# Optimization experiments

Measured on AMD Instinct MI355X. Metric: run time of the kernel, lower is better.

The kernel has to match this reference:

```python
import jax, jax.numpy as jnp
import numpy as np

N = 128  # n_hidden == n_inputs == n_outputs
TWO_PI = 2.0 * np.pi


def build_unitary(mzi_phases, output_phases):
    """Clements mesh: n layers of disjoint 2x2 MZI rotations, composed left-to-right.
    Within a layer the MZIs act on disjoint pairs, so their product equals one dense
    layer matrix (matches the sequential torch loop exactly)."""
    n = N
    U = jnp.eye(n, dtype=jnp.complex64)
    idx = 0
    for layer in range(n):
        pi = np.arange(layer % 2, n - 1, 2)  # left indices of pairs this layer
        m = len(pi)
        theta = mzi_phases[idx:idx + 2 * m:2]
        phi = mzi_phases[idx + 1:idx + 2 * m:2]
        idx += 2 * m
        ct = jnp.cos(theta).astype(jnp.complex64)
        st = jnp.sin(theta).astype(jnp.complex64)
        ep = jnp.exp(1j * phi.astype(jnp.complex64))
        L = jnp.eye(n, dtype=jnp.complex64)
        L = L.at[pi, pi].set(ct * ep)
        L = L.at[pi, pi + 1].set(st)
        L = L.at[pi + 1, pi].set(st)
        L = L.at[pi + 1, pi + 1].set(-ct * jnp.conj(ep))
        U = U @ L
    return U * jnp.exp(1j * output_phases.astype(jnp.complex64))[None, :]


def nofu(z, alpha, beta):
    eps = 1e-8
    intensity = jnp.abs(z) ** 2 + eps
    a = jnp.clip(alpha, 0.0, 10.0)
    b = jnp.clip(beta, 0.0, 10.0)
    transmission = jnp.exp(-a[None, :] / (1.0 + b[None, :] * intensity))
    return z * jnp.sqrt(transmission).astype(z.dtype)


def setup_inputs() -> dict:
    key = jax.random.key(0)
    ks = jax.random.split(key, 16)
    B = 65536
    num_mzi_phases = N * (N - 1)  # 2 phases per MZI
    inp = {
        "x": jax.random.normal(ks[0], (B, N), jnp.float32),
        "input_phases": jnp.zeros((N,), jnp.float32),
        "mzi_phases1": jax.random.uniform(ks[1], (num_mzi_phases,), jnp.float32) * TWO_PI,
        "out_phases1": jnp.zeros((N,), jnp.float32),
        "alpha1": jnp.full((N,), 0.5, jnp.float32),
        "beta1": jnp.full((N,), 0.2, jnp.float32),
        "mzi_phases2": jax.random.uniform(ks[2], (num_mzi_phases,), jnp.float32) * TWO_PI,
        "out_phases2": jnp.zeros((N,), jnp.float32),
        "alpha2": jnp.full((N,), 0.5, jnp.float32),
        "beta2": jnp.full((N,), 0.2, jnp.float32),
        "mzi_phases3": jax.random.uniform(ks[3], (num_mzi_phases,), jnp.float32) * TWO_PI,
        "out_phases3": jnp.zeros((N,), jnp.float32),
        "W": jax.random.normal(ks[4], (N, 2 * N), jnp.float32) * 0.05,  # torch Linear weight [out,in]
        "b": jnp.zeros((N,), jnp.float32),
    }
    return inp


def reference(x, input_phases, mzi_phases1, out_phases1, alpha1, beta1,
              mzi_phases2, out_phases2, alpha2, beta2,
              mzi_phases3, out_phases3, W, b):
    # Eval mode: no BatchNorm, no dropout.
    z = x.astype(jnp.complex64) * jnp.exp(1j * input_phases.astype(jnp.complex64))[None, :]
    z = z @ build_unitary(mzi_phases1, out_phases1)
    z = nofu(z, alpha1, beta1)
    z = z @ build_unitary(mzi_phases2, out_phases2)
    z = nofu(z, alpha2, beta2)
    z = z @ build_unitary(mzi_phases3, out_phases3)
    real_output = jnp.concatenate([jnp.real(z), jnp.imag(z)], axis=1)
    return real_output @ W.T + b[None, :]
```

## Files before the change

kernel.cpp:

```cpp
#include <hip/hip_runtime.h>
#include <math.h>

typedef __attribute__((ext_vector_type(8))) short bf16x8;
typedef __attribute__((ext_vector_type(4))) float f32x4;
typedef unsigned short u16;

__device__ __forceinline__ unsigned short f2bf(float f) {
    unsigned u = __builtin_bit_cast(unsigned, f);
    u += 0x7fffu + ((u >> 16) & 1u);
    return (unsigned short)(u >> 16);
}
__device__ __forceinline__ float bf2f(unsigned short v) {
    return __builtin_bit_cast(float, (unsigned)v << 16);
}

__global__ __launch_bounds__(128) void prep_all_kernel(
    const float* __restrict__ mzi1, const float* __restrict__ mzi2,
    const float* __restrict__ mzi3, const float* __restrict__ inph,
    const float* __restrict__ outph1, const float* __restrict__ outph2,
    const float* __restrict__ outph3,
    u16* __restrict__ P1, u16* __restrict__ P2, u16* __restrict__ P3)
{
    const int b = blockIdx.x, t = threadIdx.x;
    if (t >= 64) return;

    const int s = b >> 7, r = b & 127;
    const float* mzi = (s == 0) ? mzi1 : ((s == 1) ? mzi2 : mzi3);

    float2 a = make_float2(0.f, 0.f), b2 = make_float2(0.f, 0.f);
    if (s == 0) {
        float sp, cp; __sincosf(inph[r], &sp, &cp);
        if (2 * t == r)     a  = make_float2(cp, sp);
        if (2 * t + 1 == r) b2 = make_float2(cp, sp);
    } else {
        if (2 * t == r)     a.x  = 1.f;
        if (2 * t + 1 == r) b2.x = 1.f;
    }

    auto ldmz = [&](int L) -> float2 {
        const int start = L & 1;
        const int m = 64 - start;
        if (t < m) {
            const int off = (L >> 1) * 254 + start * 128 + 2 * t;
            return *(const float2*)(mzi + off);
        }
        return make_float2(0.f, 0.f);
    };
    float2 mz[4];
    #pragma unroll
    for (int i = 0; i < 4; ++i) mz[i] = ldmz(i);

    #pragma unroll 4
    for (int L = 0; L < 128; ++L) {
        const float2 v = mz[L & 3];
        if (L < 124) mz[L & 3] = ldmz(L + 4);
        float st, ct, sp, cp;
        __sincosf(v.x, &st, &ct);
        __sincosf(v.y, &sp, &cp);
        if ((L & 1) == 0) {
            float pr = ct * (a.x * cp - a.y * sp) + st * b2.x;
            float pi = ct * (a.x * sp + a.y * cp) + st * b2.y;
            float qr = st * a.x - ct * (b2.x * cp + b2.y * sp);
            float qi = st * a.y - ct * (b2.y * cp - b2.x * sp);
            a = make_float2(pr, pi); b2 = make_float2(qr, qi);
        } else {
            float2 an;
            an.x = __shfl_down(a.x, 1); an.y = __shfl_down(a.y, 1);
            float pr = ct * (b2.x * cp - b2.y * sp) + st * an.x;
            float pi = ct * (b2.x * sp + b2.y * cp) + st * an.y;
            float qr = st * b2.x - ct * (an.x * cp + an.y * sp);
            float qi = st * b2.y - ct * (an.y * cp - an.x * sp);
            if (t < 63) b2 = make_float2(pr, pi);
            float2 qs;
            qs.x = __shfl_up(qr, 1); qs.y = __shfl_up(qi, 1);
            if (t >= 1) a = qs;
        }
    }

    const float* outph = (s == 0) ? outph1 : ((s == 1) ? outph2 : outph3);
    #pragma unroll
    for (int h = 0; h < 2; ++h) {
        const int j = 2 * t + h;
        float2 w = h ? b2 : a;
        float sp, cp; __sincosf(outph[j], &sp, &cp);
        const float wr = w.x * cp - w.y * sp;
        const float wi = w.x * sp + w.y * cp;
        const int cre = ((j >> 4) * 32) + (j & 15);
        if (s == 0) {
            P1[cre * 128 + r]        = f2bf(wr);
            P1[(cre + 16) * 128 + r] = f2bf(wi);
        } else {
            u16* P = (s == 1) ? P2 : P3;
            const int rre = ((r >> 4) * 32) + (r & 15);
            P[cre * 256 + rre]             = f2bf(wr);
            P[cre * 256 + rre + 16]        = f2bf(-wi);
            P[(cre + 16) * 256 + rre]      = f2bf(wi);
            P[(cre + 16) * 256 + rre + 16] = f2bf(wr);
        }
    }
}

__global__ __launch_bounds__(256) void combine_kernel(
    const u16* __restrict__ P3, const float* __restrict__ W,
    u16* __restrict__ P34)
{
    __shared__ float partial[8][256];
    const int n  = blockIdx.x;
    const int t  = threadIdx.x;
    const int cs = t >> 5;
    const int kb = (t & 31) * 8;

    float acc[8];
    #pragma unroll
    for (int e = 0; e < 8; ++e) acc[e] = 0.f;

    #pragma unroll 4
    for (int cc = 0; cc < 32; ++cc) {
        const int c = cs * 32 + cc;
        const int j = (cc < 16) ? (cs * 16 + cc) : (128 + cs * 16 + (cc - 16));
        const float w = W[n * 256 + j];
        bf16x8 p = *(const bf16x8*)&P3[c * 256 + kb];
        #pragma unroll
        for (int e = 0; e < 8; ++e)
            acc[e] = fmaf(bf2f((unsigned short)p[e]), w, acc[e]);
    }

    #pragma unroll
    for (int e = 0; e < 8; ++e) partial[cs][kb + e] = acc[e];
    __syncthreads();

    if (cs == 0) {
        #pragma unroll
        for (int e = 0; e < 8; ++e) {
            float s = 0.f;
            #pragma unroll
            for (int q = 0; q < 8; ++q) s += partial[q][kb + e];
            P34[n * 256 + kb + e] = f2bf(s);
        }
    }
}

__global__ __launch_bounds__(512, 4) void ficonn_mfma_kernel(
    const float* __restrict__ x,
    const u16* __restrict__ P1, const u16* __restrict__ P2,
    const u16* __restrict__ P34,
    const float* __restrict__ al1, const float* __restrict__ be1,
    const float* __restrict__ al2, const float* __restrict__ be2,
    const float* __restrict__ bias, float* __restrict__ out)
{
    __shared__ __align__(16) char zBuf[2][32768];
    char* const z0 = zBuf[0];
    char* const z1 = zBuf[1];

    const int tid  = threadIdx.x;
    const int lane = tid & 63;
    const int wv   = tid >> 6;
    const int l16  = lane & 15;
    const int kg   = lane >> 4;
    const int nb   = wv * 32;
    const size_t rowBase = (size_t)blockIdx.x * 64;

    const int jf = wv * 16 + l16;
    const float av1 = 0.5f * fminf(fmaxf(al1[jf], 0.f), 10.f);
    const float bv1 = fminf(fmaxf(be1[jf], 0.f), 10.f);
    const float av2 = 0.5f * fminf(fmaxf(al2[jf], 0.f), 10.f);
    const float bv2 = fminf(fmaxf(be2[jf], 0.f), 10.f);

    {
        const float4* xg = (const float4*)(x + rowBase * 128);
        #pragma unroll
        for (int i = 0; i < 4; ++i) {
            const int idx = tid + i * 512;
            const int row = idx >> 5;
            const int c4  = idx & 31;
            float4 f = xg[idx];
            uint2 v;
            v.x = (unsigned)f2bf(f.x) | ((unsigned)f2bf(f.y) << 16);
            v.y = (unsigned)f2bf(f.z) | ((unsigned)f2bf(f.w) << 16);
            const unsigned byte = ((unsigned)(row * 512 + c4 * 8)) ^ ((unsigned)(row & 31) << 4);
            *(uint2*)(z0 + byte) = v;
        }
    }
    __syncthreads();

    f32x4 acc[4][2];

    #pragma unroll
    for (int mt = 0; mt < 4; ++mt)
        #pragma unroll
        for (int nt = 0; nt < 2; ++nt) acc[mt][nt] = (f32x4){0.f, 0.f, 0.f, 0.f};

    #pragma unroll 2
    for (int ksl = 0; ksl < 4; ++ksl) {
        const int k0 = ksl * 32 + kg * 8;
        bf16x8 A[4];
        #pragma unroll
        for (int mt = 0; mt < 4; ++mt) {
            const int row = mt * 16 + l16;
            const unsigned byte = ((unsigned)(row * 512 + k0 * 2)) ^ ((unsigned)(row & 31) << 4);
            A[mt] = *(const bf16x8*)(z0 + byte);
        }
        #pragma unroll
        for (int nt = 0; nt < 2; ++nt) {
            bf16x8 Bf = *(const bf16x8*)&P1[(nb + nt * 16 + l16) * 128 + k0];
            #pragma unroll
            for (int mt = 0; mt < 4; ++mt)
                acc[mt][nt] = __builtin_amdgcn_mfma_f32_16x16x32_bf16(A[mt], Bf, acc[mt][nt], 0, 0, 0);
        }
    }

    #pragma unroll
    for (int mt = 0; mt < 4; ++mt)
        #pragma unroll
        for (int r = 0; r < 4; ++r) {
            float re = acc[mt][0][r], im = acc[mt][1][r];
            float I = fmaf(re, re, fmaf(im, im, 1e-8f));
            float fct = __expf(__fdividef(-av1, fmaf(bv1, I, 1.f)));
            re *= fct; im *= fct;
            const int row = mt * 16 + kg * 4 + r;
            const int colRe = nb + l16;
            const unsigned sw = (unsigned)(row & 31) << 4;
            *(u16*)(z1 + (((unsigned)(row * 512 + colRe * 2)) ^ sw)) = f2bf(re);
            *(u16*)(z1 + (((unsigned)(row * 512 + (colRe + 16) * 2)) ^ sw)) = f2bf(im);
        }
    __syncthreads();

    #pragma unroll
    for (int mt = 0; mt < 4; ++mt)
        #pragma unroll
        for (int nt = 0; nt < 2; ++nt) acc[mt][nt] = (f32x4){0.f, 0.f, 0.f, 0.f};

    #pragma unroll 2
    for (int ks = 0; ks < 8; ++ks) {
        const int k0 = ks * 32 + kg * 8;
        bf16x8 A[4];
        #pragma unroll
        for (int mt = 0; mt < 4; ++mt) {
            const int row = mt * 16 + l16;
            const unsigned byte = ((unsigned)(row * 512 + k0 * 2)) ^ ((unsigned)(row & 31) << 4);
            A[mt] = *(const bf16x8*)(z1 + byte);
        }
        #pragma unroll
        for (int nt = 0; nt < 2; ++nt) {
            bf16x8 Bf = *(const bf16x8*)&P2[(nb + nt * 16 + l16) * 256 + k0];
            #pragma unroll
            for (int mt = 0; mt < 4; ++mt)
                acc[mt][nt] = __builtin_amdgcn_mfma_f32_16x16x32_bf16(A[mt], Bf, acc[mt][nt], 0, 0, 0);
        }
    }

    #pragma unroll
    for (int mt = 0; mt < 4; ++mt)
        #pragma unroll
        for (int r = 0; r < 4; ++r) {
            float re = acc[mt][0][r], im = acc[mt][1][r];
            float I = fmaf(re, re, fmaf(im, im, 1e-8f));
            float fct = __expf(__fdividef(-av2, fmaf(bv2, I, 1.f)));
            re *= fct; im *= fct;
            const int row = mt * 16 + kg * 4 + r;
            const int colRe = nb + l16;
            const unsigned sw = (unsigned)(row & 31) << 4;
            *(u16*)(z0 + (((unsigned)(row * 512 + colRe * 2)) ^ sw)) = f2bf(re);
            *(u16*)(z0 + (((unsigned)(row * 512 + (colRe + 16) * 2)) ^ sw)) = f2bf(im);
        }
    __syncthreads();

    f32x4 facc[4];
    #pragma unroll
    for (int mt = 0; mt < 4; ++mt) facc[mt] = (f32x4){0.f, 0.f, 0.f, 0.f};

    const int nb2 = wv * 16;
    #pragma unroll 2
    for (int ks = 0; ks < 8; ++ks) {
        const int k0 = ks * 32 + kg * 8;
        bf16x8 A[4];
        #pragma unroll
        for (int mt = 0; mt < 4; ++mt) {
            const int row = mt * 16 + l16;
            const unsigned byte = ((unsigned)(row * 512 + k0 * 2)) ^ ((unsigned)(row & 31) << 4);
            A[mt] = *(const bf16x8*)(z0 + byte);
        }
        bf16x8 Bf = *(const bf16x8*)&P34[(nb2 + l16) * 256 + k0];
        #pragma unroll
        for (int mt = 0; mt < 4; ++mt)
            facc[mt] = __builtin_amdgcn_mfma_f32_16x16x32_bf16(A[mt], Bf, facc[mt], 0, 0, 0);
    }

    const float bcol = bias[nb2 + l16];
    #pragma unroll
    for (int mt = 0; mt < 4; ++mt)
        #pragma unroll
        for (int r = 0; r < 4; ++r) {
            const size_t row = rowBase + mt * 16 + kg * 4 + r;
            out[row * 128 + nb2 + l16] = facc[mt][r] + bcol;
        }
}

extern "C" void kernel_launch(void* const* d_in, const int* in_sizes, int n_in,
                              void* d_out, int out_size, void* d_ws, size_t ws_size,
                              hipStream_t stream)
{
    const float* x      = (const float*)d_in[0];
    const float* inph   = (const float*)d_in[1];
    const float* mzi1   = (const float*)d_in[2];
    const float* outph1 = (const float*)d_in[3];
    const float* alpha1 = (const float*)d_in[4];
    const float* beta1  = (const float*)d_in[5];
    const float* mzi2   = (const float*)d_in[6];
    const float* outph2 = (const float*)d_in[7];
    const float* alpha2 = (const float*)d_in[8];
    const float* beta2  = (const float*)d_in[9];
    const float* mzi3   = (const float*)d_in[10];
    const float* outph3 = (const float*)d_in[11];
    const float* W      = (const float*)d_in[12];
    const float* bias   = (const float*)d_in[13];

    const int B = in_sizes[0] / 128;

    u16* P1  = (u16*)d_ws;
    u16* P2  = P1 + 32768;
    u16* P3  = P2 + 65536;
    u16* P34 = P3 + 65536;

    prep_all_kernel<<<384, 128, 0, stream>>>(
        mzi1, mzi2, mzi3, inph, outph1, outph2, outph3, P1, P2, P3);
    combine_kernel<<<128, 256, 0, stream>>>(P3, W, P34);
    ficonn_mfma_kernel<<<B / 64, 512, 0, stream>>>(
        x, P1, P2, P34, alpha1, beta1, alpha2, beta2, bias, (float*)d_out);
}
```

Measured before the change: 75.48 us.

## Split fused MFMA pipeline into three stage kernels staging activations through global memory

```diff
diff --git a/kernel.cpp b/kernel.cpp
--- a/kernel.cpp
+++ b/kernel.cpp
@@ -89,13 +89,17 @@
         if (s == 0) {
             P1[cre * 128 + r]        = f2bf(wr);
             P1[(cre + 16) * 128 + r] = f2bf(wi);
+        } else if (s == 1) {
+            P2[cre * 256 + 2 * r]            = f2bf(wr);
+            P2[cre * 256 + 2 * r + 1]        = f2bf(-wi);
+            P2[(cre + 16) * 256 + 2 * r]     = f2bf(wi);
+            P2[(cre + 16) * 256 + 2 * r + 1] = f2bf(wr);
         } else {
-            u16* P = (s == 1) ? P2 : P3;
             const int rre = ((r >> 4) * 32) + (r & 15);
-            P[cre * 256 + rre]             = f2bf(wr);
-            P[cre * 256 + rre + 16]        = f2bf(-wi);
-            P[(cre + 16) * 256 + rre]      = f2bf(wi);
-            P[(cre + 16) * 256 + rre + 16] = f2bf(wr);
+            P3[cre * 256 + rre]             = f2bf(wr);
+            P3[cre * 256 + rre + 16]        = f2bf(-wi);
+            P3[(cre + 16) * 256 + rre]      = f2bf(wi);
+            P3[(cre + 16) * 256 + rre + 16] = f2bf(wr);
         }
     }
 }
@@ -135,22 +139,23 @@
             float s = 0.f;
             #pragma unroll
             for (int q = 0; q < 8; ++q) s += partial[q][kb + e];
-            P34[n * 256 + kb + e] = f2bf(s);
-        }
-    }
-}
-
-__global__ __launch_bounds__(512, 4) void ficonn_mfma_kernel(
-    const float* __restrict__ x,
-    const u16* __restrict__ P1, const u16* __restrict__ P2,
-    const u16* __restrict__ P34,
+            const int k = kb + e;
+            const int g = k >> 5, i = k & 31;
+            const int rf = g * 16 + (i & 15);
+            P34[n * 256 + 2 * rf + (i >> 4)] = f2bf(s);
+        }
+    }
+}
+
+
+__global__ __launch_bounds__(512, 4) void stage1_kernel(
+    const float* __restrict__ x, const u16* __restrict__ P1,
     const float* __restrict__ al1, const float* __restrict__ be1,
-    const float* __restrict__ al2, const float* __restrict__ be2,
-    const float* __restrict__ bias, float* __restrict__ out)
-{
-    __shared__ __align__(16) char zBuf[2][32768];
-    char* const z0 = zBuf[0];
-    char* const z1 = zBuf[1];
+    u16* z)
+{
+    __shared__ __align__(16) char zA[32768];
+    (void)zA;
+    __shared__ __align__(16) char xT[16384];
 
     const int tid  = threadIdx.x;
     const int lane = tid & 63;
@@ -163,8 +168,6 @@
     const int jf = wv * 16 + l16;
     const float av1 = 0.5f * fminf(fmaxf(al1[jf], 0.f), 10.f);
     const float bv1 = fminf(fmaxf(be1[jf], 0.f), 10.f);
-    const float av2 = 0.5f * fminf(fmaxf(al2[jf], 0.f), 10.f);
-    const float bv2 = fminf(fmaxf(be2[jf], 0.f), 10.f);
 
     {
         const float4* xg = (const float4*)(x + rowBase * 128);
@@ -177,14 +180,13 @@
             uint2 v;
             v.x = (unsigned)f2bf(f.x) | ((unsigned)f2bf(f.y) << 16);
             v.y = (unsigned)f2bf(f.z) | ((unsigned)f2bf(f.w) << 16);
-            const unsigned byte = ((unsigned)(row * 512 + c4 * 8)) ^ ((unsigned)(row & 31) << 4);
-            *(uint2*)(z0 + byte) = v;
+            const unsigned byte = ((unsigned)(row * 256 + c4 * 8)) ^ ((unsigned)(row & 15) << 4);
+            *(uint2*)(xT + byte) = v;
         }
     }
     __syncthreads();
 
     f32x4 acc[4][2];
-
     #pragma unroll
     for (int mt = 0; mt < 4; ++mt)
         #pragma unroll
@@ -197,8 +199,8 @@
         #pragma unroll
         for (int mt = 0; mt < 4; ++mt) {
             const int row = mt * 16 + l16;
-            const unsigned byte = ((unsigned)(row * 512 + k0 * 2)) ^ ((unsigned)(row & 31) << 4);
-            A[mt] = *(const bf16x8*)(z0 + byte);
+            const unsigned byte = ((unsigned)(row * 256 + k0 * 2)) ^ ((unsigned)(row & 15) << 4);
+            A[mt] = *(const bf16x8*)(xT + byte);
         }
         #pragma unroll
         for (int nt = 0; nt < 2; ++nt) {
@@ -217,14 +219,46 @@
             float I = fmaf(re, re, fmaf(im, im, 1e-8f));
             float fct = __expf(__fdividef(-av1, fmaf(bv1, I, 1.f)));
             re *= fct; im *= fct;
-            const int row = mt * 16 + kg * 4 + r;
-            const int colRe = nb + l16;
-            const unsigned sw = (unsigned)(row & 31) << 4;
-            *(u16*)(z1 + (((unsigned)(row * 512 + colRe * 2)) ^ sw)) = f2bf(re);
-            *(u16*)(z1 + (((unsigned)(row * 512 + (colRe + 16) * 2)) ^ sw)) = f2bf(im);
-        }
+            unsigned pk = (unsigned)f2bf(re) | ((unsigned)f2bf(im) << 16);
+            const size_t row = rowBase + mt * 16 + kg * 4 + r;
+            *(unsigned*)(z + row * 256 + 2 * jf) = pk;
+        }
+}
+
+__global__ __launch_bounds__(512, 4) void stage2_kernel(
+    const u16* zin, const u16* __restrict__ P2,
+    const float* __restrict__ al2, const float* __restrict__ be2,
+    u16* zout)
+{
+    __shared__ __align__(16) char zA[32768];
+
+    const int tid  = threadIdx.x;
+    const int lane = tid & 63;
+    const int wv   = tid >> 6;
+    const int l16  = lane & 15;
+    const int kg   = lane >> 4;
+    const int nb   = wv * 32;
+    const size_t rowBase = (size_t)blockIdx.x * 64;
+
+    const int jf = wv * 16 + l16;
+    const float av2 = 0.5f * fminf(fmaxf(al2[jf], 0.f), 10.f);
+    const float bv2 = fminf(fmaxf(be2[jf], 0.f), 10.f);
+
+    {
+        const uint4* zg = (const uint4*)(zin + rowBase * 256);
+        #pragma unroll
+        for (int i = 0; i < 4; ++i) {
+            const int idx = tid + i * 512;
+            const int row = idx >> 5;
+            const int c16 = idx & 31;
+            uint4 v = zg[idx];
+            const unsigned byte = ((unsigned)(row * 512 + c16 * 16)) ^ ((unsigned)(row & 31) << 4);
+            *(uint4*)(zA + byte) = v;
+        }
+    }
     __syncthreads();
 
+    f32x4 acc[4][2];
     #pragma unroll
     for (int mt = 0; mt < 4; ++mt)
         #pragma unroll
@@ -238,7 +272,7 @@
         for (int mt = 0; mt < 4; ++mt) {
             const int row = mt * 16 + l16;
             const unsigned byte = ((unsigned)(row * 512 + k0 * 2)) ^ ((unsigned)(row & 31) << 4);
-            A[mt] = *(const bf16x8*)(z1 + byte);
+            A[mt] = *(const bf16x8*)(zA + byte);
         }
         #pragma unroll
         for (int nt = 0; nt < 2; ++nt) {
@@ -257,12 +291,37 @@
             float I = fmaf(re, re, fmaf(im, im, 1e-8f));
             float fct = __expf(__fdividef(-av2, fmaf(bv2, I, 1.f)));
             re *= fct; im *= fct;
-            const int row = mt * 16 + kg * 4 + r;
-            const int colRe = nb + l16;
-            const unsigned sw = (unsigned)(row & 31) << 4;
-            *(u16*)(z0 + (((unsigned)(row * 512 + colRe * 2)) ^ sw)) = f2bf(re);
-            *(u16*)(z0 + (((unsigned)(row * 512 + (colRe + 16) * 2)) ^ sw)) = f2bf(im);
-        }
+            unsigned pk = (unsigned)f2bf(re) | ((unsigned)f2bf(im) << 16);
+            const size_t row = rowBase + mt * 16 + kg * 4 + r;
+            *(unsigned*)(zout + row * 256 + 2 * jf) = pk;
+        }
+}
+
+__global__ __launch_bounds__(512, 4) void final_kernel(
+    const u16* zin, const u16* __restrict__ P34,
+    const float* __restrict__ bias, float* out)
+{
+    __shared__ __align__(16) char zA[32768];
+
+    const int tid  = threadIdx.x;
+    const int lane = tid & 63;
+    const int wv   = tid >> 6;
+    const int l16  = lane & 15;
+    const int kg   = lane >> 4;
+    const size_t rowBase = (size_t)blockIdx.x * 64;
+
+    {
+        const uint4* zg = (const uint4*)(zin + rowBase * 256);
+        #pragma unroll
+        for (int i = 0; i < 4; ++i) {
+            const int idx = tid + i * 512;
+            const int row = idx >> 5;
+            const int c16 = idx & 31;
+            uint4 v = zg[idx];
+            const unsigned byte = ((unsigned)(row * 512 + c16 * 16)) ^ ((unsigned)(row & 31) << 4);
+            *(uint4*)(zA + byte) = v;
+        }
+    }
     __syncthreads();
 
     f32x4 facc[4];
@@ -278,7 +337,7 @@
         for (int mt = 0; mt < 4; ++mt) {
             const int row = mt * 16 + l16;
             const unsigned byte = ((unsigned)(row * 512 + k0 * 2)) ^ ((unsigned)(row & 31) << 4);
-            A[mt] = *(const bf16x8*)(z0 + byte);
+            A[mt] = *(const bf16x8*)(zA + byte);
         }
         bf16x8 Bf = *(const bf16x8*)&P34[(nb2 + l16) * 256 + k0];
         #pragma unroll
@@ -322,9 +381,12 @@
     u16* P3  = P2 + 65536;
     u16* P34 = P3 + 65536;
 
+    u16* zbuf = (u16*)d_out;
+
     prep_all_kernel<<<384, 128, 0, stream>>>(
         mzi1, mzi2, mzi3, inph, outph1, outph2, outph3, P1, P2, P3);
     combine_kernel<<<128, 256, 0, stream>>>(P3, W, P34);
-    ficonn_mfma_kernel<<<B / 64, 512, 0, stream>>>(
-        x, P1, P2, P34, alpha1, beta1, alpha2, beta2, bias, (float*)d_out);
-}
+    stage1_kernel<<<B / 64, 512, 0, stream>>>(x, P1, alpha1, beta1, zbuf);
+    stage2_kernel<<<B / 64, 512, 0, stream>>>(zbuf, P2, alpha2, beta2, zbuf);
+    final_kernel<<<B / 64, 512, 0, stream>>>(zbuf, P34, bias, (float*)d_out);
+}
```

Result: slower. 91.49 us (+21.2%).
